# Optimization experiments

Measured on AMD Instinct MI355X. Metric: run time of the kernel, lower is better.

The kernel has to match this reference:

```python
import jax, jax.numpy as jnp
import numpy as np

K = 7
PAD = K // 2
C = 24          # latent_dim
ITERS = 4


def conv2d(x, w, b):
    # x: (B, Cin, H, W), w: (Cout, Cin, kh, kw) -> (B, Cout, H, W), SAME padding
    y = jax.lax.conv_general_dilated(
        x, w, window_strides=(1, 1), padding='SAME',
        dimension_numbers=('NCHW', 'OIHW', 'NCHW'))
    return y + b[None, :, None, None]


def unfold(x, H, W):
    # F.unfold(x, K, padding=PAD).view(B, C, K*K, H, W)
    # ordering: for each channel, kernel offsets row-major (kh outer, kw inner)
    xp = jnp.pad(x, ((0, 0), (0, 0), (PAD, PAD), (PAD, PAD)))
    patches = jnp.stack(
        [xp[:, :, i:i + H, j:j + W] for i in range(K) for j in range(K)],
        axis=2)  # (B, C, K*K, H, W)
    return patches


def setup_inputs() -> dict:
    key = jax.random.key(0)
    ks = jax.random.split(key, 8)
    B, H, W = 2, 256, 256
    depth = jax.random.normal(ks[0], (B, 1, H, W), dtype=jnp.float32)
    texture = jax.random.normal(ks[1], (B, 3, H, W), dtype=jnp.float32)
    # depth_proj: Conv2d(1, C, 3, padding=1)
    w_dp = jax.random.normal(ks[2], (C, 1, 3, 3), dtype=jnp.float32) * 0.1
    b_dp = jax.random.normal(ks[3], (C,), dtype=jnp.float32) * 0.1
    # kernel_predictor: Conv2d(3, C*K*K, 3, padding=1) followed by softmax(dim=1)
    w_kp = jax.random.normal(ks[4], (C * K * K, 3, 3, 3), dtype=jnp.float32) * 0.1
    b_kp = jax.random.normal(ks[5], (C * K * K,), dtype=jnp.float32) * 0.1
    # to_depth: Conv2d(C, 1, 1)
    w_td = jax.random.normal(ks[6], (1, C, 1, 1), dtype=jnp.float32) * 0.1
    b_td = jax.random.normal(ks[7], (1,), dtype=jnp.float32) * 0.1
    return {'depth': depth, 'texture': texture,
            'w_dp': w_dp, 'b_dp': b_dp,
            'w_kp': w_kp, 'b_kp': b_kp,
            'w_td': w_td, 'b_td': b_td}


def reference(depth, texture, w_dp, b_dp, w_kp, b_kp, w_td, b_td):
    B, _, H, W = depth.shape
    depth_latent = conv2d(depth, w_dp, b_dp)                    # (B, C, H, W)
    logits = conv2d(texture, w_kp, b_kp)                        # (B, C*K*K, H, W)
    kernels = jax.nn.softmax(logits, axis=1)                    # softmax over full channel dim
    kernels = kernels.reshape(B, C, K * K, H, W)
    unfolded = unfold(depth_latent, H, W)                       # (B, C, K*K, H, W)
    for it in range(ITERS):
        diffused = jnp.sum(kernels * unfolded, axis=2)          # (B, C, H, W)
        if it < ITERS - 1:
            unfolded = unfold(diffused, H, W)
    fused_depth = conv2d(diffused, w_td, b_td)                  # (B, 1, H, W)
    return fused_depth
```

## Files before the change

kernel.cpp:

```cpp
#include <hip/hip_runtime.h>

#define BB   2
#define HH   256
#define WW   256
#define HWSZ (HH * WW)
#define CC   24
#define KSZ  7
#define KK   49
#define PADK 3
#define G    8
#define CPG  3
#define LSTR 24
#define CSTR (22 * LSTR)
#define LOG2E 1.44269504088896340736f

typedef __attribute__((ext_vector_type(8))) short short8;
typedef __attribute__((ext_vector_type(4))) float float4v;

__device__ __forceinline__ short f2bf(float x) {
  unsigned u = __builtin_bit_cast(unsigned, x);
  unsigned r = u + 0x7FFFu + ((u >> 16) & 1u);
  return (short)(r >> 16);
}
__device__ __forceinline__ float bf2f(short h) {
  unsigned u = ((unsigned)(unsigned short)h) << 16;
  return __builtin_bit_cast(float, u);
}

__global__ __launch_bounds__(256) void k_setup(
    const float* __restrict__ w_kp, const float* __restrict__ b_kp,
    const float* __restrict__ tex, short* __restrict__ wsW,
    short* __restrict__ wsB) {
  __shared__ float lt[3 * 324];
  __shared__ int lltk[32];
  int blk = blockIdx.x;
  if (blk < 192) {
    int s = blk & 1, mt = (blk >> 1) & 3, cg = blk >> 3;
    for (int idx = threadIdx.x; idx < 640; idx += 256) {
      int row = idx / 40, k = idx % 40;
      int kk = mt * 16 + row;
      float v = 0.f;
      if (kk < KK && k < 28)
        v = ((k < 27) ? w_kp[((size_t)cg * KK + kk) * 27 + k]
                      : b_kp[cg * KK + kk]) * LOG2E;
      short hi = f2bf(v);
      short h = (s == 0) ? hi : f2bf(v - bf2f(hi));
      wsW[(size_t)blk * 640 + idx] = h;
    }
    return;
  }
  int tb = blk - 192;
  int b = tb >> 8, tile = tb & 255;
  int y0 = (tile >> 4) * 16, x0 = (tile & 15) * 16;
  int tid = threadIdx.x, lane = tid & 63, wv = tid >> 6;
  int q = lane >> 4, col = lane & 15;

  if (tid < 32) {
    int k = tid, v;
    if (k < 27) v = (k / 9) * 324 + ((k % 9) / 3) * 18 + (k % 3);
    else if (k == 27) v = -1;
    else v = -2;
    lltk[k] = v;
  }
  for (int idx = tid; idx < 972; idx += 256) {
    int ci = idx / 324, r = idx % 324;
    int iy = r / 18, ix = r % 18;
    int yy = y0 + iy - 1, xx = x0 + ix - 1;
    bool ok = (yy >= 0 && yy < HH && xx >= 0 && xx < WW);
    lt[idx] = ok ? tex[((size_t)b * 3 + ci) * HWSZ + yy * WW + xx] : 0.f;
  }
  __syncthreads();

  int tko[8];
#pragma unroll
  for (int j = 0; j < 8; ++j) tko[j] = lltk[q * 8 + j];
  int4* w4 = (int4*)wsB;
#pragma unroll
  for (int nt = 0; nt < 4; ++nt) {
    short8 hi, lo;
#pragma unroll
    for (int j = 0; j < 8; ++j) {
      int o = tko[j];
      float v = (o == -1) ? 1.f
                          : ((o == -2) ? 0.f : lt[o + (wv * 4 + nt) * 18 + col]);
      short h = f2bf(v);
      hi[j] = h;
      lo[j] = f2bf(v - bf2f(h));
    }
    size_t base = ((((size_t)(b * 256 + tile) * 4 + wv) * 4 + nt) * 2);
    w4[(base + 0) * 64 + lane] = __builtin_bit_cast(int4, hi);
    w4[(base + 1) * 64 + lane] = __builtin_bit_cast(int4, lo);
  }
}

template <bool FIRST, bool FINAL>
__global__ __launch_bounds__(256, 6) void k_diffuse_m(
    const float* __restrict__ depth, const float* __restrict__ src,
    const float* __restrict__ invZ, const float* __restrict__ w_dp,
    const float* __restrict__ b_dp, const short* __restrict__ wsW,
    const short* __restrict__ wsB, float* __restrict__ dst,
    float* __restrict__ part, const float* __restrict__ w_td,
    float* __restrict__ outp) {
  __shared__ float lsrc[CPG * CSTR];
  __shared__ float ldp[576];
  __shared__ int loffs[64];

  int b = blockIdx.z / G, g = blockIdx.z % G, c0 = g * CPG;
  int x0 = blockIdx.x * 16, y0 = blockIdx.y * 16;
  int tile = blockIdx.y * 16 + blockIdx.x;
  int tid = threadIdx.x, lane = tid & 63, wv = tid >> 6;
  int q = lane >> 4, col = lane & 15;

  if (tid < 64)
    loffs[tid] = (tid < KK) ? ((tid / 7) - 3) * LSTR + ((tid % 7) - 3) : 0;
  if (FIRST) {
    for (int idx = tid; idx < 576; idx += 256) {
      int iy = idx / 24, ix = idx % 24;
      int yy = y0 + iy - 4, xx = x0 + ix - 4;
      bool ok = (yy >= 0 && yy < HH && xx >= 0 && xx < WW);
      ldp[idx] = ok ? depth[(size_t)b * HWSZ + yy * WW + xx] : 0.f;
    }
  }
  __syncthreads();

  for (int idx = tid; idx < 484; idx += 256) {
    int iy = idx / 22, ix = idx % 22;
    int yy = y0 + iy - PADK, xx = x0 + ix - PADK;
    bool ok = (yy >= 0 && yy < HH && xx >= 0 && xx < WW);
    if (FIRST) {
#pragma unroll
      for (int c = 0; c < CPG; ++c) {
        float a = b_dp[c0 + c];
#pragma unroll
        for (int dy = 0; dy < 3; ++dy)
#pragma unroll
          for (int dx = 0; dx < 3; ++dx)
            a = fmaf(w_dp[(c0 + c) * 9 + dy * 3 + dx],
                     ldp[(iy + dy) * 24 + (ix + dx)], a);
        lsrc[c * CSTR + iy * LSTR + ix] = ok ? a : 0.f;
      }
    } else {
      float sc = ok ? invZ[b * HWSZ + yy * WW + xx] : 0.f;
#pragma unroll
      for (int c = 0; c < CPG; ++c)
        lsrc[c * CSTR + iy * LSTR + ix] =
            ok ? src[((size_t)b * CC + c0 + c) * HWSZ + yy * WW + xx] * sc : 0.f;
    }
  }
  __syncthreads();

  const int4* wB = (const int4*)wsB + ((size_t)(b * 256 + tile) * 4 + wv) * 512;

#pragma unroll 1
  for (int np = 0; np < 2; ++np) {
    short8 Bh0 = __builtin_bit_cast(short8, wB[(np * 4 + 0) * 64 + lane]);
    short8 Bl0 = __builtin_bit_cast(short8, wB[(np * 4 + 1) * 64 + lane]);
    short8 Bh1 = __builtin_bit_cast(short8, wB[(np * 4 + 2) * 64 + lane]);
    short8 Bl1 = __builtin_bit_cast(short8, wB[(np * 4 + 3) * 64 + lane]);
    int basep = (wv * 4 + np * 2 + 3) * LSTR + col + 3;
    float zacc[2] = {0.f, 0.f}, res[2] = {0.f, 0.f};
    float accc[2] = {0.f, 0.f};

    const short* wp = wsW + (size_t)g * 15360 + col * 40 + q * 8;
    short8 nAh = *(const short8*)wp;
    short8 nAl = *(const short8*)(wp + 640);
#pragma unroll 1
    for (int idx = 0; idx < 12; ++idx) {
      short8 Ah = nAh, Al = nAl;
      if (idx < 11) {
        wp += 1280;
        nAh = *(const short8*)wp;
        nAl = *(const short8*)(wp + 640);
      }
      int c = idx >> 2, mt = idx & 3;
      int mtb = mt * 16 + q * 4;
      const float* lsc = lsrc + c * CSTR + basep;
      int o0 = loffs[mtb + 0], o1 = loffs[mtb + 1];
      int o2 = loffs[mtb + 2], o3 = loffs[mtb + 3];
      float t00 = lsc[o0], t01 = lsc[o0 + LSTR];
      float t10 = lsc[o1], t11 = lsc[o1 + LSTR];
      float t20 = lsc[o2], t21 = lsc[o2 + LSTR];
      float t30 = lsc[o3], t31 = lsc[o3 + LSTR];

      float4v C0 = {0.f, 0.f, 0.f, 0.f}, C1 = {0.f, 0.f, 0.f, 0.f};
      C0 = __builtin_amdgcn_mfma_f32_16x16x32_bf16(Ah, Bh0, C0, 0, 0, 0);
      C1 = __builtin_amdgcn_mfma_f32_16x16x32_bf16(Ah, Bh1, C1, 0, 0, 0);
      C0 = __builtin_amdgcn_mfma_f32_16x16x32_bf16(Ah, Bl0, C0, 0, 0, 0);
      C1 = __builtin_amdgcn_mfma_f32_16x16x32_bf16(Ah, Bl1, C1, 0, 0, 0);
      C0 = __builtin_amdgcn_mfma_f32_16x16x32_bf16(Al, Bh0, C0, 0, 0, 0);
      C1 = __builtin_amdgcn_mfma_f32_16x16x32_bf16(Al, Bh1, C1, 0, 0, 0);

      if (mt < 3) {
        float e00 = __builtin_amdgcn_exp2f(C0[0]);
        float e01 = __builtin_amdgcn_exp2f(C0[1]);
        float e02 = __builtin_amdgcn_exp2f(C0[2]);
        float e03 = __builtin_amdgcn_exp2f(C0[3]);
        float e10 = __builtin_amdgcn_exp2f(C1[0]);
        float e11 = __builtin_amdgcn_exp2f(C1[1]);
        float e12 = __builtin_amdgcn_exp2f(C1[2]);
        float e13 = __builtin_amdgcn_exp2f(C1[3]);
        if (FIRST) {
          zacc[0] += (e00 + e01) + (e02 + e03);
          zacc[1] += (e10 + e11) + (e12 + e13);
        }
        float a0 = accc[0], a1 = accc[1];
        a0 = fmaf(e00, t00, a0); a1 = fmaf(e10, t01, a1);
        a0 = fmaf(e01, t10, a0); a1 = fmaf(e11, t11, a1);
        a0 = fmaf(e02, t20, a0); a1 = fmaf(e12, t21, a1);
        a0 = fmaf(e03, t30, a0); a1 = fmaf(e13, t31, a1);
        accc[0] = a0; accc[1] = a1;
      } else {
        float e0 = (q == 0) ? __builtin_amdgcn_exp2f(C0[0]) : 0.f;
        float e1 = (q == 0) ? __builtin_amdgcn_exp2f(C1[0]) : 0.f;
        if (FIRST) { zacc[0] += e0; zacc[1] += e1; }
        accc[0] = fmaf(e0, t00, accc[0]);
        accc[1] = fmaf(e1, t01, accc[1]);
      }
      if (mt == 3) {
#pragma unroll
        for (int t = 0; t < 2; ++t) {
          float v = accc[t];
          v += __shfl_xor(v, 16, 64);
          v += __shfl_xor(v, 32, 64);
          if (FINAL) {
            res[t] = fmaf(w_td[c0 + c], v, res[t]);
          } else {
            int p = (y0 + wv * 4 + np * 2 + t) * WW + (x0 + col);
            if (lane < 16) dst[((size_t)b * CC + c0 + c) * HWSZ + p] = v;
          }
          accc[t] = 0.f;
        }
      }
    }
#pragma unroll
    for (int t = 0; t < 2; ++t) {
      int p = (y0 + wv * 4 + np * 2 + t) * WW + (x0 + col);
      if (FIRST) {
        float z = zacc[t];
        z += __shfl_xor(z, 16, 64);
        z += __shfl_xor(z, 32, 64);
        if (lane < 16) part[(size_t)g * BB * HWSZ + b * HWSZ + p] = z;
      }
      if (FINAL) {
        if (lane < 16) {
          float iz = invZ[b * HWSZ + p];
          atomicAdd(&outp[(size_t)b * HWSZ + p], res[t] * iz);
        }
      }
    }
  }
}

__global__ __launch_bounds__(256) void k_zred(const float* __restrict__ zpart,
                                              float* __restrict__ invZ,
                                              const float* __restrict__ b_td,
                                              float* __restrict__ outp) {
  int t = blockIdx.x * 256 + threadIdx.x;
  float z = 0.f;
#pragma unroll
  for (int g = 0; g < G; ++g) z += zpart[(size_t)g * BB * HWSZ + t];
  invZ[t] = 1.f / z;
  outp[t] = b_td[0];
}

extern "C" void kernel_launch(void* const* d_in, const int* in_sizes, int n_in,
                              void* d_out, int out_size, void* d_ws, size_t ws_size,
                              hipStream_t stream) {
  const float* depth = (const float*)d_in[0];
  const float* tex   = (const float*)d_in[1];
  const float* w_dp  = (const float*)d_in[2];
  const float* b_dp  = (const float*)d_in[3];
  const float* w_kp  = (const float*)d_in[4];
  const float* b_kp  = (const float*)d_in[5];
  const float* w_td  = (const float*)d_in[6];
  const float* b_td  = (const float*)d_in[7];
  float* out = (float*)d_out;

  char* ws = (char*)d_ws;
  const size_t buf_b = (size_t)BB * CC * HWSZ * 4;
  float* bufA = (float*)ws;
  float* bufB = (float*)(ws + buf_b);
  float* part = (float*)(ws + 2 * buf_b);
  float* invZ = (float*)(ws + 2 * buf_b + (size_t)G * BB * HWSZ * 4);
  short* wsW  = (short*)(ws + 2 * buf_b + (size_t)G * BB * HWSZ * 4 +
                         (size_t)BB * HWSZ * 4);
  short* wsB  = (short*)(ws + 2 * buf_b + (size_t)G * BB * HWSZ * 4 +
                         (size_t)BB * HWSZ * 4 + 192 * 640 * 2);

  k_setup<<<dim3(192 + 512), dim3(256), 0, stream>>>(w_kp, b_kp, tex, wsW, wsB);

  dim3 grid(WW / 16, HH / 16, BB * G), blk(256);
  dim3 grid1(BB * HWSZ / 256), blk1(256);

  k_diffuse_m<true, false><<<grid, blk, 0, stream>>>(
      depth, nullptr, nullptr, w_dp, b_dp, wsW, wsB, bufB, part, w_td, nullptr);
  k_zred<<<grid1, blk1, 0, stream>>>(part, invZ, b_td, out);
  k_diffuse_m<false, false><<<grid, blk, 0, stream>>>(
      depth, bufB, invZ, w_dp, b_dp, wsW, wsB, bufA, part, w_td, nullptr);
  k_diffuse_m<false, false><<<grid, blk, 0, stream>>>(
      depth, bufA, invZ, w_dp, b_dp, wsW, wsB, bufB, part, w_td, nullptr);
  k_diffuse_m<false, true><<<grid, blk, 0, stream>>>(
      depth, bufB, invZ, w_dp, b_dp, wsW, wsB, nullptr, part, w_td, out);
}
```

Baseline: 296.1 us.

## Stage kernel-predictor weights in LDS and process four rows per wave

After: 435.6 us. +47.1%, slower.

```diff
diff --git a/kernel.cpp b/kernel.cpp
--- a/kernel.cpp
+++ b/kernel.cpp
@@ -36,8 +36,8 @@
   int blk = blockIdx.x;
   if (blk < 192) {
     int s = blk & 1, mt = (blk >> 1) & 3, cg = blk >> 3;
-    for (int idx = threadIdx.x; idx < 640; idx += 256) {
-      int row = idx / 40, k = idx % 40;
+    for (int idx = threadIdx.x; idx < 512; idx += 256) {
+      int row = idx >> 5, k = idx & 31;
       int kk = mt * 16 + row;
       float v = 0.f;
       if (kk < KK && k < 28)
@@ -45,7 +45,7 @@
                       : b_kp[cg * KK + kk]) * LOG2E;
       short hi = f2bf(v);
       short h = (s == 0) ? hi : f2bf(v - bf2f(hi));
-      wsW[(size_t)blk * 640 + idx] = h;
+      wsW[(size_t)blk * 512 + idx] = h;
     }
     return;
   }
@@ -94,15 +94,16 @@
 }
 
 template <bool FIRST, bool FINAL>
-__global__ __launch_bounds__(256, 6) void k_diffuse_m(
+__global__ __launch_bounds__(256, 4) void k_diffuse_m(
     const float* __restrict__ depth, const float* __restrict__ src,
     const float* __restrict__ invZ, const float* __restrict__ w_dp,
     const float* __restrict__ b_dp, const short* __restrict__ wsW,
     const short* __restrict__ wsB, float* __restrict__ dst,
     float* __restrict__ part, const float* __restrict__ w_td,
     float* __restrict__ outp) {
+  __shared__ __align__(16) short lw[24 * 512];
   __shared__ float lsrc[CPG * CSTR];
-  __shared__ float ldp[576];
+  __shared__ float ldp[FIRST ? 576 : 4];
   __shared__ int loffs[64];
 
   int b = blockIdx.z / G, g = blockIdx.z % G, c0 = g * CPG;
@@ -113,6 +114,12 @@
 
   if (tid < 64)
     loffs[tid] = (tid < KK) ? ((tid / 7) - 3) * LSTR + ((tid % 7) - 3) : 0;
+  {
+    const int4* s4 = (const int4*)(wsW + (size_t)g * 12288);
+    int4* d4 = (int4*)lw;
+#pragma unroll
+    for (int i = 0; i < 6; ++i) d4[tid + i * 256] = s4[tid + i * 256];
+  }
   if (FIRST) {
     for (int idx = tid; idx < 576; idx += 256) {
       int iy = idx / 24, ix = idx % 24;
@@ -121,6 +128,13 @@
       ldp[idx] = ok ? depth[(size_t)b * HWSZ + yy * WW + xx] : 0.f;
     }
   }
+  const int4* wB = (const int4*)wsB + ((size_t)(b * 256 + tile) * 4 + wv) * 512;
+  short8 Bh[4], Bl[4];
+#pragma unroll
+  for (int u = 0; u < 4; ++u) {
+    Bh[u] = __builtin_bit_cast(short8, wB[(u * 2 + 0) * 64 + lane]);
+    Bl[u] = __builtin_bit_cast(short8, wB[(u * 2 + 1) * 64 + lane]);
+  }
   __syncthreads();
 
   for (int idx = tid; idx < 484; idx += 256) {
@@ -149,103 +163,96 @@
   }
   __syncthreads();
 
-  const int4* wB = (const int4*)wsB + ((size_t)(b * 256 + tile) * 4 + wv) * 512;
+  const float* tp[16];
+  {
+    const float* basep = lsrc + (wv * 4 + 3) * LSTR + col + 3;
+#pragma unroll
+    for (int j = 0; j < 16; ++j)
+      tp[j] = basep + loffs[(j >> 2) * 16 + q * 4 + (j & 3)];
+  }
+
+  float accc[4] = {0.f, 0.f, 0.f, 0.f};
+  float zacc[4] = {0.f, 0.f, 0.f, 0.f};
+  float res[4]  = {0.f, 0.f, 0.f, 0.f};
+  const short* lA = lw + col * 32 + q * 8;
 
 #pragma unroll 1
-  for (int np = 0; np < 2; ++np) {
-    short8 Bh0 = __builtin_bit_cast(short8, wB[(np * 4 + 0) * 64 + lane]);
-    short8 Bl0 = __builtin_bit_cast(short8, wB[(np * 4 + 1) * 64 + lane]);
-    short8 Bh1 = __builtin_bit_cast(short8, wB[(np * 4 + 2) * 64 + lane]);
-    short8 Bl1 = __builtin_bit_cast(short8, wB[(np * 4 + 3) * 64 + lane]);
-    int basep = (wv * 4 + np * 2 + 3) * LSTR + col + 3;
-    float zacc[2] = {0.f, 0.f}, res[2] = {0.f, 0.f};
-    float accc[2] = {0.f, 0.f};
-
-    const short* wp = wsW + (size_t)g * 15360 + col * 40 + q * 8;
-    short8 nAh = *(const short8*)wp;
-    short8 nAl = *(const short8*)(wp + 640);
-#pragma unroll 1
-    for (int idx = 0; idx < 12; ++idx) {
-      short8 Ah = nAh, Al = nAl;
-      if (idx < 11) {
-        wp += 1280;
-        nAh = *(const short8*)wp;
-        nAl = *(const short8*)(wp + 640);
-      }
-      int c = idx >> 2, mt = idx & 3;
-      int mtb = mt * 16 + q * 4;
-      const float* lsc = lsrc + c * CSTR + basep;
-      int o0 = loffs[mtb + 0], o1 = loffs[mtb + 1];
-      int o2 = loffs[mtb + 2], o3 = loffs[mtb + 3];
-      float t00 = lsc[o0], t01 = lsc[o0 + LSTR];
-      float t10 = lsc[o1], t11 = lsc[o1 + LSTR];
-      float t20 = lsc[o2], t21 = lsc[o2 + LSTR];
-      float t30 = lsc[o3], t31 = lsc[o3 + LSTR];
-
-      float4v C0 = {0.f, 0.f, 0.f, 0.f}, C1 = {0.f, 0.f, 0.f, 0.f};
-      C0 = __builtin_amdgcn_mfma_f32_16x16x32_bf16(Ah, Bh0, C0, 0, 0, 0);
-      C1 = __builtin_amdgcn_mfma_f32_16x16x32_bf16(Ah, Bh1, C1, 0, 0, 0);
-      C0 = __builtin_amdgcn_mfma_f32_16x16x32_bf16(Ah, Bl0, C0, 0, 0, 0);
-      C1 = __builtin_amdgcn_mfma_f32_16x16x32_bf16(Ah, Bl1, C1, 0, 0, 0);
-      C0 = __builtin_amdgcn_mfma_f32_16x16x32_bf16(Al, Bh0, C0, 0, 0, 0);
-      C1 = __builtin_amdgcn_mfma_f32_16x16x32_bf16(Al, Bh1, C1, 0, 0, 0);
-
+  for (int c = 0; c < CPG; ++c) {
+#pragma unroll
+    for (int mt = 0; mt < 4; ++mt) {
+      short8 Ah = *(const short8*)(lA + (mt * 2 + 0) * 512);
+      short8 Al = *(const short8*)(lA + (mt * 2 + 1) * 512);
+      float tv[16];
+#pragma unroll
+      for (int j = 0; j < 4; ++j) {
+        const float* t = tp[mt * 4 + j];
+#pragma unroll
+        for (int u = 0; u < 4; ++u) tv[j * 4 + u] = t[u * LSTR];
+      }
+      float4v C[4];
+#pragma unroll
+      for (int u = 0; u < 4; ++u) {
+        float4v Cu = {0.f, 0.f, 0.f, 0.f};
+        Cu = __builtin_amdgcn_mfma_f32_16x16x32_bf16(Ah, Bh[u], Cu, 0, 0, 0);
+        Cu = __builtin_amdgcn_mfma_f32_16x16x32_bf16(Ah, Bl[u], Cu, 0, 0, 0);
+        Cu = __builtin_amdgcn_mfma_f32_16x16x32_bf16(Al, Bh[u], Cu, 0, 0, 0);
+        C[u] = Cu;
+      }
       if (mt < 3) {
-        float e00 = __builtin_amdgcn_exp2f(C0[0]);
-        float e01 = __builtin_amdgcn_exp2f(C0[1]);
-        float e02 = __builtin_amdgcn_exp2f(C0[2]);
-        float e03 = __builtin_amdgcn_exp2f(C0[3]);
-        float e10 = __builtin_amdgcn_exp2f(C1[0]);
-        float e11 = __builtin_amdgcn_exp2f(C1[1]);
-        float e12 = __builtin_amdgcn_exp2f(C1[2]);
-        float e13 = __builtin_amdgcn_exp2f(C1[3]);
-        if (FIRST) {
-          zacc[0] += (e00 + e01) + (e02 + e03);
-          zacc[1] += (e10 + e11) + (e12 + e13);
+#pragma unroll
+        for (int u = 0; u < 4; ++u) {
+          float e0 = __builtin_amdgcn_exp2f(C[u][0]);
+          float e1 = __builtin_amdgcn_exp2f(C[u][1]);
+          float e2 = __builtin_amdgcn_exp2f(C[u][2]);
+          float e3 = __builtin_amdgcn_exp2f(C[u][3]);
+          if (FIRST) zacc[u] += (e0 + e1) + (e2 + e3);
+          float a = accc[u];
+          a = fmaf(e0, tv[0 * 4 + u], a);
+          a = fmaf(e1, tv[1 * 4 + u], a);
+          a = fmaf(e2, tv[2 * 4 + u], a);
+          a = fmaf(e3, tv[3 * 4 + u], a);
+          accc[u] = a;
         }
-        float a0 = accc[0], a1 = accc[1];
-        a0 = fmaf(e00, t00, a0); a1 = fmaf(e10, t01, a1);
-        a0 = fmaf(e01, t10, a0); a1 = fmaf(e11, t11, a1);
-        a0 = fmaf(e02, t20, a0); a1 = fmaf(e12, t21, a1);
-        a0 = fmaf(e03, t30, a0); a1 = fmaf(e13, t31, a1);
-        accc[0] = a0; accc[1] = a1;
       } else {
-        float e0 = (q == 0) ? __builtin_amdgcn_exp2f(C0[0]) : 0.f;
-        float e1 = (q == 0) ? __builtin_amdgcn_exp2f(C1[0]) : 0.f;
-        if (FIRST) { zacc[0] += e0; zacc[1] += e1; }
-        accc[0] = fmaf(e0, t00, accc[0]);
-        accc[1] = fmaf(e1, t01, accc[1]);
-      }
-      if (mt == 3) {
-#pragma unroll
-        for (int t = 0; t < 2; ++t) {
-          float v = accc[t];
-          v += __shfl_xor(v, 16, 64);
-          v += __shfl_xor(v, 32, 64);
-          if (FINAL) {
-            res[t] = fmaf(w_td[c0 + c], v, res[t]);
-          } else {
-            int p = (y0 + wv * 4 + np * 2 + t) * WW + (x0 + col);
-            if (lane < 16) dst[((size_t)b * CC + c0 + c) * HWSZ + p] = v;
-          }
-          accc[t] = 0.f;
+#pragma unroll
+        for (int u = 0; u < 4; ++u) {
+          float e = (q == 0) ? __builtin_amdgcn_exp2f(C[u][0]) : 0.f;
+          if (FIRST) zacc[u] += e;
+          accc[u] = fmaf(e, tv[0 * 4 + u], accc[u]);
         }
       }
     }
 #pragma unroll
-    for (int t = 0; t < 2; ++t) {
-      int p = (y0 + wv * 4 + np * 2 + t) * WW + (x0 + col);
-      if (FIRST) {
-        float z = zacc[t];
-        z += __shfl_xor(z, 16, 64);
-        z += __shfl_xor(z, 32, 64);
-        if (lane < 16) part[(size_t)g * BB * HWSZ + b * HWSZ + p] = z;
-      }
+    for (int u = 0; u < 4; ++u) {
+      float v = accc[u];
+      v += __shfl_xor(v, 16, 64);
+      v += __shfl_xor(v, 32, 64);
       if (FINAL) {
-        if (lane < 16) {
-          float iz = invZ[b * HWSZ + p];
-          atomicAdd(&outp[(size_t)b * HWSZ + p], res[t] * iz);
-        }
+        res[u] = fmaf(w_td[c0 + c], v, res[u]);
+      } else {
+        int p = (y0 + wv * 4 + u) * WW + (x0 + col);
+        if (lane < 16) dst[((size_t)b * CC + c0 + c) * HWSZ + p] = v;
+      }
+      accc[u] = 0.f;
+    }
+    lA += 4096;
+#pragma unroll
+    for (int j = 0; j < 16; ++j) tp[j] += CSTR;
+  }
+
+#pragma unroll
+  for (int u = 0; u < 4; ++u) {
+    int p = (y0 + wv * 4 + u) * WW + (x0 + col);
+    if (FIRST) {
+      float z = zacc[u];
+      z += __shfl_xor(z, 16, 64);
+      z += __shfl_xor(z, 32, 64);
+      if (lane < 16) part[(size_t)g * BB * HWSZ + b * HWSZ + p] = z;
+    }
+    if (FINAL) {
+      if (lane < 16) {
+        float iz = invZ[b * HWSZ + p];
+        atomicAdd(&outp[(size_t)b * HWSZ + p], res[u] * iz);
       }
     }
   }
@@ -285,7 +292,7 @@
   short* wsW  = (short*)(ws + 2 * buf_b + (size_t)G * BB * HWSZ * 4 +
                          (size_t)BB * HWSZ * 4);
   short* wsB  = (short*)(ws + 2 * buf_b + (size_t)G * BB * HWSZ * 4 +
-                         (size_t)BB * HWSZ * 4 + 192 * 640 * 2);
+                         (size_t)BB * HWSZ * 4 + 192 * 512 * 2);
 
   k_setup<<<dim3(192 + 512), dim3(256), 0, stream>>>(w_kp, b_kp, tex, wsW, wsB);
 
```

## Stage kernel-predictor weights in LDS and shrink padded weight layout

Applied to the files above, without the earlier changes.

After: 280.6 us. 5.2% less time.

```diff
diff --git a/kernel.cpp b/kernel.cpp
--- a/kernel.cpp
+++ b/kernel.cpp
@@ -36,8 +36,8 @@
   int blk = blockIdx.x;
   if (blk < 192) {
     int s = blk & 1, mt = (blk >> 1) & 3, cg = blk >> 3;
-    for (int idx = threadIdx.x; idx < 640; idx += 256) {
-      int row = idx / 40, k = idx % 40;
+    for (int idx = threadIdx.x; idx < 512; idx += 256) {
+      int row = idx >> 5, k = idx & 31;
       int kk = mt * 16 + row;
       float v = 0.f;
       if (kk < KK && k < 28)
@@ -45,7 +45,7 @@
                       : b_kp[cg * KK + kk]) * LOG2E;
       short hi = f2bf(v);
       short h = (s == 0) ? hi : f2bf(v - bf2f(hi));
-      wsW[(size_t)blk * 640 + idx] = h;
+      wsW[(size_t)blk * 512 + idx] = h;
     }
     return;
   }
@@ -94,15 +94,16 @@
 }
 
 template <bool FIRST, bool FINAL>
-__global__ __launch_bounds__(256, 6) void k_diffuse_m(
+__global__ __launch_bounds__(256, 4) void k_diffuse_m(
     const float* __restrict__ depth, const float* __restrict__ src,
     const float* __restrict__ invZ, const float* __restrict__ w_dp,
     const float* __restrict__ b_dp, const short* __restrict__ wsW,
     const short* __restrict__ wsB, float* __restrict__ dst,
     float* __restrict__ part, const float* __restrict__ w_td,
     float* __restrict__ outp) {
+  __shared__ __align__(16) short lw[24 * 512];
   __shared__ float lsrc[CPG * CSTR];
-  __shared__ float ldp[576];
+  __shared__ float ldp[FIRST ? 576 : 4];
   __shared__ int loffs[64];
 
   int b = blockIdx.z / G, g = blockIdx.z % G, c0 = g * CPG;
@@ -113,6 +114,12 @@
 
   if (tid < 64)
     loffs[tid] = (tid < KK) ? ((tid / 7) - 3) * LSTR + ((tid % 7) - 3) : 0;
+  {
+    const int4* s4 = (const int4*)(wsW + (size_t)g * 12288);
+    int4* d4 = (int4*)lw;
+#pragma unroll
+    for (int i = 0; i < 6; ++i) d4[tid + i * 256] = s4[tid + i * 256];
+  }
   if (FIRST) {
     for (int idx = tid; idx < 576; idx += 256) {
       int iy = idx / 24, ix = idx % 24;
@@ -161,26 +168,19 @@
     float zacc[2] = {0.f, 0.f}, res[2] = {0.f, 0.f};
     float accc[2] = {0.f, 0.f};
 
-    const short* wp = wsW + (size_t)g * 15360 + col * 40 + q * 8;
-    short8 nAh = *(const short8*)wp;
-    short8 nAl = *(const short8*)(wp + 640);
+    const short* lAp = lw + col * 32 + q * 8;
 #pragma unroll 1
     for (int idx = 0; idx < 12; ++idx) {
-      short8 Ah = nAh, Al = nAl;
-      if (idx < 11) {
-        wp += 1280;
-        nAh = *(const short8*)wp;
-        nAl = *(const short8*)(wp + 640);
-      }
+      short8 Ah = *(const short8*)(lAp);
+      short8 Al = *(const short8*)(lAp + 512);
+      lAp += 1024;
       int c = idx >> 2, mt = idx & 3;
       int mtb = mt * 16 + q * 4;
       const float* lsc = lsrc + c * CSTR + basep;
-      int o0 = loffs[mtb + 0], o1 = loffs[mtb + 1];
-      int o2 = loffs[mtb + 2], o3 = loffs[mtb + 3];
-      float t00 = lsc[o0], t01 = lsc[o0 + LSTR];
-      float t10 = lsc[o1], t11 = lsc[o1 + LSTR];
-      float t20 = lsc[o2], t21 = lsc[o2 + LSTR];
-      float t30 = lsc[o3], t31 = lsc[o3 + LSTR];
+      const float* p0 = lsc + loffs[mtb + 0];
+      const float* p1 = lsc + loffs[mtb + 1];
+      const float* p2 = lsc + loffs[mtb + 2];
+      const float* p3 = lsc + loffs[mtb + 3];
 
       float4v C0 = {0.f, 0.f, 0.f, 0.f}, C1 = {0.f, 0.f, 0.f, 0.f};
       C0 = __builtin_amdgcn_mfma_f32_16x16x32_bf16(Ah, Bh0, C0, 0, 0, 0);
@@ -204,17 +204,17 @@
           zacc[1] += (e10 + e11) + (e12 + e13);
         }
         float a0 = accc[0], a1 = accc[1];
-        a0 = fmaf(e00, t00, a0); a1 = fmaf(e10, t01, a1);
-        a0 = fmaf(e01, t10, a0); a1 = fmaf(e11, t11, a1);
-        a0 = fmaf(e02, t20, a0); a1 = fmaf(e12, t21, a1);
-        a0 = fmaf(e03, t30, a0); a1 = fmaf(e13, t31, a1);
+        a0 = fmaf(e00, p0[0], a0); a1 = fmaf(e10, p0[LSTR], a1);
+        a0 = fmaf(e01, p1[0], a0); a1 = fmaf(e11, p1[LSTR], a1);
+        a0 = fmaf(e02, p2[0], a0); a1 = fmaf(e12, p2[LSTR], a1);
+        a0 = fmaf(e03, p3[0], a0); a1 = fmaf(e13, p3[LSTR], a1);
         accc[0] = a0; accc[1] = a1;
       } else {
         float e0 = (q == 0) ? __builtin_amdgcn_exp2f(C0[0]) : 0.f;
         float e1 = (q == 0) ? __builtin_amdgcn_exp2f(C1[0]) : 0.f;
         if (FIRST) { zacc[0] += e0; zacc[1] += e1; }
-        accc[0] = fmaf(e0, t00, accc[0]);
-        accc[1] = fmaf(e1, t01, accc[1]);
+        accc[0] = fmaf(e0, p0[0], accc[0]);
+        accc[1] = fmaf(e1, p0[LSTR], accc[1]);
       }
       if (mt == 3) {
 #pragma unroll
@@ -285,7 +285,7 @@
   short* wsW  = (short*)(ws + 2 * buf_b + (size_t)G * BB * HWSZ * 4 +
                          (size_t)BB * HWSZ * 4);
   short* wsB  = (short*)(ws + 2 * buf_b + (size_t)G * BB * HWSZ * 4 +
-                         (size_t)BB * HWSZ * 4 + 192 * 640 * 2);
+                         (size_t)BB * HWSZ * 4 + 192 * 512 * 2);
 
   k_setup<<<dim3(192 + 512), dim3(256), 0, stream>>>(w_kp, b_kp, tex, wsW, wsB);
 
```
